# Kernel optimization log

Hardware: AMD Instinct MI355X
Metric: run time of the kernel (lower is better)

Reference implementation:

```python
import jax, jax.numpy as jnp
import numpy as np

B, L, C, N, D, FF, L2 = 1, 2400, 1536, 12, 128, 8960, 512
F_, H_, W_ = 2, 30, 40  # grid: L = F*H*W
EPS = 1e-6


def _rope_table(max_len=1024, d=D):
    # Wan rope_params: three bands of sizes d-4*(d//6), 2*(d//6), 2*(d//6)
    parts = [d - 4 * (d // 6), 2 * (d // 6), 2 * (d // 6)]
    pos = np.arange(max_len, dtype=np.float32)
    cs, ss = [], []
    for dp in parts:
        inv = 1.0 / (10000.0 ** (np.arange(0, dp, 2, dtype=np.float32) / dp))
        ang = np.outer(pos, inv)
        cs.append(np.cos(ang)); ss.append(np.sin(ang))
    return np.stack([np.concatenate(cs, 1), np.concatenate(ss, 1)], -1)  # [1024, d//2, 2]


def setup_inputs() -> dict:
    key = jax.random.key(0)
    ks = iter(jax.random.split(key, 48))
    def rn(shape, s=0.02):
        return jax.random.normal(next(ks), shape, dtype=jnp.float32) * s
    inp = dict(
        x=jax.random.normal(next(ks), (B, L, C), dtype=jnp.float32),
        e=rn((B, 1, 6, C), 0.5),
        context=jax.random.normal(next(ks), (B, L2, C), dtype=jnp.float32),
        freqs=jnp.asarray(_rope_table()),
        seq_lens=jnp.full((B,), L, dtype=jnp.int32),
        context_lens=jnp.full((B,), L2, dtype=jnp.int32),
        grid_sizes=jnp.array([[F_, H_, W_]], dtype=jnp.int32),
        modulation=rn((1, 6, C), 0.5),
    )
    for p in ('sa', 'ca'):
        for w in ('q', 'k', 'v', 'o'):
            inp[f'{p}_{w}_w'] = rn((C, C))
            inp[f'{p}_{w}_b'] = rn((C,))
        inp[f'{p}_nq_w'] = jnp.ones((C,), jnp.float32)
        inp[f'{p}_nk_w'] = jnp.ones((C,), jnp.float32)
    inp['ffn_w1'] = rn((C, FF)); inp['ffn_b1'] = rn((FF,))
    inp['ffn_w2'] = rn((FF, C)); inp['ffn_b2'] = rn((C,))
    return inp


def _rms_norm(x, w):
    v = jnp.mean(jnp.square(x), axis=-1, keepdims=True)
    return x * jax.lax.rsqrt(v + EPS) * w


def _layer_norm(x):
    m = jnp.mean(x, axis=-1, keepdims=True)
    v = jnp.mean(jnp.square(x - m), axis=-1, keepdims=True)
    return (x - m) * jax.lax.rsqrt(v + EPS)


def _apply_rope(x, freqs):
    # x: [B,S,N,D]; freqs: [1024, D//2, 2] (cos, sin). Wan default rope.
    c = D // 2
    p0, p1 = c - 2 * (c // 3), c // 3
    ft = jnp.broadcast_to(freqs[:F_, None, None, :p0], (F_, H_, W_, p0, 2))
    fh = jnp.broadcast_to(freqs[None, :H_, None, p0:p0 + p1], (F_, H_, W_, p1, 2))
    fw = jnp.broadcast_to(freqs[None, None, :W_, p0 + p1:], (F_, H_, W_, c - p0 - p1, 2))
    fr = jnp.concatenate([ft, fh, fw], axis=3).reshape(L, c, 2)
    cos = fr[..., 0][None, :, None, :]  # [1,S,1,c]
    sin = fr[..., 1][None, :, None, :]
    xp = x.reshape(B, x.shape[1], N, c, 2)  # interleaved (real, imag) pairs
    xr, xi = xp[..., 0], xp[..., 1]
    out = jnp.stack([xr * cos - xi * sin, xr * sin + xi * cos], axis=-1)
    return out.reshape(x.shape)


def _attention(q, k, v, k_len):
    # q:[B,Sq,N,D] k,v:[B,Sk,N,D]; dense softmax attention with k_lens mask
    scale = 1.0 / jnp.sqrt(jnp.float32(D))
    scores = jnp.einsum('bqnd,bknd->bnqk', q, k) * scale
    mask = jnp.arange(k.shape[1])[None, None, None, :] < k_len[:, None, None, None]
    scores = jnp.where(mask, scores, -jnp.inf)
    p = jax.nn.softmax(scores, axis=-1)
    return jnp.einsum('bnqk,bknd->bqnd', p, v)


def reference(x, e, context, freqs, seq_lens, context_lens, grid_sizes, modulation,
              sa_q_w, sa_q_b, sa_k_w, sa_k_b, sa_v_w, sa_v_b, sa_o_w, sa_o_b, sa_nq_w, sa_nk_w,
              ca_q_w, ca_q_b, ca_k_w, ca_k_b, ca_v_w, ca_v_b, ca_o_w, ca_o_b, ca_nq_w, ca_nk_w,
              ffn_w1, ffn_b1, ffn_w2, ffn_b2):
    # e: [B,1,6,C] (L1=1, broadcast over L == repeat_e); modulation: [1,6,C]
    em = modulation[None] + e  # [B,1,6,C]
    e0, e1, e2, e3, e4, e5 = (em[:, :, i] for i in range(6))  # each [B,1,C]
    # --- self attention with modulation ---
    h = e0 + _layer_norm(x) * (1.0 + e1)
    q = _rms_norm(h @ sa_q_w + sa_q_b, sa_nq_w).reshape(B, L, N, D)
    k = _rms_norm(h @ sa_k_w + sa_k_b, sa_nk_w).reshape(B, L, N, D)
    v = (h @ sa_v_w + sa_v_b).reshape(B, L, N, D)
    q = _apply_rope(q, freqs)
    k = _apply_rope(k, freqs)
    y = _attention(q, k, v, seq_lens).reshape(B, L, C)
    y = y @ sa_o_w + sa_o_b
    x = x + y * e2
    # --- cross attention (norm3 = Identity, cross_attn_norm=False) ---
    q = _rms_norm(x @ ca_q_w + ca_q_b, ca_nq_w).reshape(B, L, N, D)
    k = _rms_norm(context @ ca_k_w + ca_k_b, ca_nk_w).reshape(B, L2, N, D)
    v = (context @ ca_v_w + ca_v_b).reshape(B, L2, N, D)
    y = _attention(q, k, v, context_lens).reshape(B, L, C)
    x = x + (y @ ca_o_w + ca_o_b)
    # --- FFN with modulation ---
    h = e3 + _layer_norm(x) * (1.0 + e4)
    y = jax.nn.gelu(h @ ffn_w1 + ffn_b1, approximate=True) @ ffn_w2 + ffn_b2
    x = x + y * e5
    return x
```

## Files before the change

### kernel.cpp

```cpp
#include <hip/hip_runtime.h>
#include <cstddef>
#include <cstdint>

#define C_DIM   1536
#define L_SEQ   2400
#define L_CTX   512
#define N_HEADS 12
#define D_HEAD  128
#define FF_DIM  8960
#define F_GRID  2
#define H_GRID  30
#define W_GRID  40
#define EPS_F   1e-6f

#define ROPE_P0 22
#define ROPE_P1 43

typedef __attribute__((ext_vector_type(8))) short short8;
typedef __attribute__((ext_vector_type(4))) float f32x4;

__device__ inline unsigned short f2bf(float f) {
    union { float f; unsigned int u; } v; v.f = f;
    unsigned int r = v.u + 0x7FFF + ((v.u >> 16) & 1);
    return (unsigned short)(r >> 16);
}

#define GL2LDS(gp, lp) \
    __builtin_amdgcn_global_load_lds((const __attribute__((address_space(1))) void*)(gp), \
                                     (__attribute__((address_space(3))) void*)(lp), 16, 0, 0)


__global__ __launch_bounds__(256) void k_embed(const float* __restrict__ mod,
                                               const float* __restrict__ e,
                                               float* __restrict__ ev, int n) {
    int i = blockIdx.x * 256 + threadIdx.x;
    if (i < n) ev[i] = mod[i] + e[i];
}

__global__ __launch_bounds__(256) void k_resid2(const float* __restrict__ a,
                                                const float* __restrict__ b,
                                                const float* __restrict__ ev, int ei,
                                                float* __restrict__ out,
                                                unsigned short* __restrict__ outb, int n) {
    int i = (blockIdx.x * 256 + threadIdx.x) * 2;
    if (i >= n) return;
    int c = i % C_DIM;
    float s0 = 1.f, s1 = 1.f;
    if (ei >= 0) {
        s0 = ev[ei * C_DIM + c];
        s1 = ev[ei * C_DIM + c + 1];
    }
    float2 av = *(const float2*)(a + i);
    float2 bv = *(const float2*)(b + i);
    float o0 = av.x + bv.x * s0;
    float o1 = av.y + bv.y * s1;
    *(float2*)(out + i) = make_float2(o0, o1);
    if (outb) {
        unsigned int pk = (unsigned int)f2bf(o0) | ((unsigned int)f2bf(o1) << 16);
        *(unsigned int*)(outb + i) = pk;
    }
}

__global__ __launch_bounds__(256) void k_tobf(const float* __restrict__ X,
                                              unsigned short* __restrict__ Y, int n) {
    int i = (blockIdx.x * 256 + threadIdx.x) * 2;
    if (i >= n) return;
    float2 v = *(const float2*)(X + i);
    unsigned int pk = (unsigned int)f2bf(v.x) | ((unsigned int)f2bf(v.y) << 16);
    *(unsigned int*)(Y + i) = pk;
}

__global__ __launch_bounds__(256) void k_lnmod_bf16(const float* __restrict__ X,
                                                    const float* __restrict__ ev,
                                                    int i0, int i1,
                                                    unsigned short* __restrict__ H) {
    __shared__ float rs[256];
    __shared__ float rs2[256];
    int row = blockIdx.x, tid = threadIdx.x;
    const float* xr = X + (size_t)row * C_DIM;
    float2 vals[3];
    float s = 0.f, s2 = 0.f;
#pragma unroll
    for (int i = 0; i < 3; ++i) {
        float2 v = *(const float2*)(xr + 2 * (tid + 256 * i));
        vals[i] = v;
        s += v.x + v.y; s2 += v.x * v.x + v.y * v.y;
    }
    rs[tid] = s; rs2[tid] = s2;
    __syncthreads();
    for (int st = 128; st > 0; st >>= 1) {
        if (tid < st) { rs[tid] += rs[tid + st]; rs2[tid] += rs2[tid + st]; }
        __syncthreads();
    }
    float mean = rs[0] * (1.0f / C_DIM);
    float var  = rs2[0] * (1.0f / C_DIM) - mean * mean;
    float rinv = rsqrtf(var + EPS_F);
    const float* E0 = ev + (size_t)i0 * C_DIM;
    const float* E1 = ev + (size_t)i1 * C_DIM;
    unsigned short* hr = H + (size_t)row * C_DIM;
#pragma unroll
    for (int i = 0; i < 3; ++i) {
        int c = 2 * (tid + 256 * i);
        float o0 = E0[c]     + (vals[i].x - mean) * rinv * (1.0f + E1[c]);
        float o1 = E0[c + 1] + (vals[i].y - mean) * rinv * (1.0f + E1[c + 1]);
        unsigned int pk = (unsigned int)f2bf(o0) | ((unsigned int)f2bf(o1) << 16);
        *(unsigned int*)(hr + c) = pk;
    }
}

__global__ __launch_bounds__(256) void k_rms_rope_bf16(const float* __restrict__ X,
                                                       const float* __restrict__ w,
                                                       const float* __restrict__ freqs,
                                                       int do_rope, float outscale,
                                                       unsigned short* __restrict__ Y) {
    __shared__ float rs[256];
    int row = blockIdx.x, tid = threadIdx.x;
    const float* xr = X + (size_t)row * C_DIM;
    float2 vals[3];
    float ss = 0.f;
#pragma unroll
    for (int i = 0; i < 3; ++i) {
        int p = tid + 256 * i;
        float2 v = *(const float2*)(xr + 2 * p);
        vals[i] = v;
        ss += v.x * v.x + v.y * v.y;
    }
    rs[tid] = ss;
    __syncthreads();
    for (int st = 128; st > 0; st >>= 1) {
        if (tid < st) rs[tid] += rs[tid + st];
        __syncthreads();
    }
    float rinv = rsqrtf(rs[0] * (1.0f / C_DIM) + EPS_F);
    int f = row / (H_GRID * W_GRID);
    int rem = row % (H_GRID * W_GRID);
    int hh = rem / W_GRID, ww = rem % W_GRID;
    unsigned short* yr = Y + (size_t)row * C_DIM;
#pragma unroll
    for (int i = 0; i < 3; ++i) {
        int p = tid + 256 * i;
        int c = 2 * p;
        float a = vals[i].x * rinv * w[c];
        float b = vals[i].y * rinv * w[c + 1];
        if (do_rope) {
            int j = p & 63;
            int idx = (j < ROPE_P0) ? f : (j < ROPE_P1) ? hh : ww;
            float cv = freqs[(idx * 64 + j) * 2 + 0];
            float sv = freqs[(idx * 64 + j) * 2 + 1];
            float na = a * cv - b * sv;
            float nb = a * sv + b * cv;
            a = na; b = nb;
        }
        a *= outscale; b *= outscale;
        unsigned int pk = (unsigned int)f2bf(a) | ((unsigned int)f2bf(b) << 16);
        *(unsigned int*)(yr + c) = pk;
    }
}

__global__ __launch_bounds__(256) void k_wt(const float* __restrict__ W,
                                            unsigned short* __restrict__ WT,
                                            int K, int N) {
    __shared__ float tile[32][33];
    int k0 = blockIdx.x * 32, n0 = blockIdx.y * 32;
    int t = threadIdx.x;
    int r = t >> 3, c4 = (t & 7) * 4;
    float4 v = *(const float4*)(W + (size_t)(k0 + r) * N + n0 + c4);
    tile[r][c4 + 0] = v.x; tile[r][c4 + 1] = v.y;
    tile[r][c4 + 2] = v.z; tile[r][c4 + 3] = v.w;
    __syncthreads();
    int n = t >> 3, k4 = (t & 7) * 4;
    uint2 o;
    o.x = (unsigned int)f2bf(tile[k4 + 0][n]) | ((unsigned int)f2bf(tile[k4 + 1][n]) << 16);
    o.y = (unsigned int)f2bf(tile[k4 + 2][n]) | ((unsigned int)f2bf(tile[k4 + 3][n]) << 16);
    *(uint2*)(WT + (size_t)(n0 + n) * K + k0 + k4) = o;
}

__global__ __launch_bounds__(256) void k_vt(const float* __restrict__ V,
                                            unsigned short* __restrict__ Vt, int Lk) {
    __shared__ float tile[32][33];
    int k0 = blockIdx.x * 32, h = blockIdx.y, d0 = blockIdx.z * 32;
    int t = threadIdx.x;
    int k = t >> 3, d4 = (t & 7) * 4;
    float4 v = *(const float4*)(V + (size_t)(k0 + k) * C_DIM + h * D_HEAD + d0 + d4);
    tile[k][d4 + 0] = v.x; tile[k][d4 + 1] = v.y;
    tile[k][d4 + 2] = v.z; tile[k][d4 + 3] = v.w;
    __syncthreads();
    int d = t >> 3, k4 = (t & 7) * 4;
    uint2 o;
    o.x = (unsigned int)f2bf(tile[k4 + 0][d]) | ((unsigned int)f2bf(tile[k4 + 1][d]) << 16);
    o.y = (unsigned int)f2bf(tile[k4 + 2][d]) | ((unsigned int)f2bf(tile[k4 + 3][d]) << 16);
    *(uint2*)(Vt + (size_t)(h * D_HEAD + d0 + d) * Lk + k0 + k4) = o;
}

__global__ __launch_bounds__(256) void k_attn_mfma(const unsigned short* __restrict__ Qb,
                                                   const unsigned short* __restrict__ Kb,
                                                   const unsigned short* __restrict__ Vt,
                                                   unsigned short* __restrict__ O,
                                                   int Lq, int Lk) {
    __shared__ __align__(16) unsigned short Ks[32][136];
    __shared__ __align__(16) unsigned short Vs[128][40];
    __shared__ __align__(16) unsigned short Ps[4][16][40];
    const int tid = threadIdx.x;
    const int w = tid >> 6, lane = tid & 63;
    const int ln = lane & 15, lq = lane >> 4;
    const int h = blockIdx.y;
    const int q0 = blockIdx.x * 64 + w * 16;
    int qrow = q0 + ln; if (qrow >= Lq) qrow = Lq - 1;
    short8 qf[4];
#pragma unroll
    for (int c = 0; c < 4; ++c)
        qf[c] = *(const short8*)(Qb + (size_t)qrow * C_DIM + h * D_HEAD + c * 32 + lq * 8);
    f32x4 oacc[8];
#pragma unroll
    for (int t = 0; t < 8; ++t) oacc[t] = (f32x4){0.f, 0.f, 0.f, 0.f};
    float m_run[4] = {-3e38f, -3e38f, -3e38f, -3e38f};
    float l_run[4] = {0.f, 0.f, 0.f, 0.f};
    const float LOG2E = 1.4426950408889634f;

    for (int kb = 0; kb < Lk; kb += 32) {
        __syncthreads();
#pragma unroll
        for (int i = 0; i < 2; ++i) {
            int id = tid + i * 256;
            int r = id >> 4, c = id & 15;
            *(uint4*)&Ks[r][c * 8] =
                *(const uint4*)(Kb + (size_t)(kb + r) * C_DIM + h * D_HEAD + c * 8);
            int d = id >> 2, c2 = id & 3;
            *(uint4*)&Vs[d][c2 * 8] =
                *(const uint4*)(Vt + (size_t)(h * D_HEAD + d) * Lk + kb + c2 * 8);
        }
        __syncthreads();
        f32x4 c0 = (f32x4){0.f, 0.f, 0.f, 0.f};
        f32x4 c1 = (f32x4){0.f, 0.f, 0.f, 0.f};
#pragma unroll
        for (int c = 0; c < 4; ++c) {
            short8 b0 = *(const short8*)&Ks[ln][c * 32 + lq * 8];
            short8 b1 = *(const short8*)&Ks[16 + ln][c * 32 + lq * 8];
            c0 = __builtin_amdgcn_mfma_f32_16x16x32_bf16(qf[c], b0, c0, 0, 0, 0);
            c1 = __builtin_amdgcn_mfma_f32_16x16x32_bf16(qf[c], b1, c1, 0, 0, 0);
        }
        float alpha[4];
#pragma unroll
        for (int r = 0; r < 4; ++r) {
            float mx = fmaxf(c0[r], c1[r]);
            mx = fmaxf(mx, __shfl_xor(mx, 1));
            mx = fmaxf(mx, __shfl_xor(mx, 2));
            mx = fmaxf(mx, __shfl_xor(mx, 4));
            mx = fmaxf(mx, __shfl_xor(mx, 8));
            float mn = fmaxf(m_run[r], mx);
            alpha[r] = exp2f((m_run[r] - mn) * LOG2E);
            float p0 = exp2f((c0[r] - mn) * LOG2E);
            float p1 = exp2f((c1[r] - mn) * LOG2E);
            float s = p0 + p1;
            s += __shfl_xor(s, 1);
            s += __shfl_xor(s, 2);
            s += __shfl_xor(s, 4);
            s += __shfl_xor(s, 8);
            l_run[r] = l_run[r] * alpha[r] + s;
            m_run[r] = mn;
            Ps[w][lq * 4 + r][ln] = f2bf(p0);
            Ps[w][lq * 4 + r][16 + ln] = f2bf(p1);
        }
#pragma unroll
        for (int t = 0; t < 8; ++t)
#pragma unroll
            for (int r = 0; r < 4; ++r) oacc[t][r] *= alpha[r];
        short8 pa = *(const short8*)&Ps[w][ln][lq * 8];
#pragma unroll
        for (int t = 0; t < 8; ++t) {
            short8 bv = *(const short8*)&Vs[t * 16 + ln][lq * 8];
            oacc[t] = __builtin_amdgcn_mfma_f32_16x16x32_bf16(pa, bv, oacc[t], 0, 0, 0);
        }
    }
    float linv[4];
#pragma unroll
    for (int r = 0; r < 4; ++r) linv[r] = 1.0f / l_run[r];
#pragma unroll
    for (int t = 0; t < 8; ++t)
#pragma unroll
        for (int r = 0; r < 4; ++r) {
            int row = q0 + lq * 4 + r;
            if (row < Lq)
                O[(size_t)row * C_DIM + h * D_HEAD + t * 16 + ln] = f2bf(oacc[t][r] * linv[r]);
        }
}

__global__ __launch_bounds__(256) void k_gemm_bf16(const unsigned short* __restrict__ A,
                                                   const unsigned short* __restrict__ BT,
                                                   const float* __restrict__ bias,
                                                   float* __restrict__ Cf,
                                                   unsigned short* __restrict__ Cb,
                                                   int M, int N, int K, int gelu) {
    __shared__ __align__(16) unsigned short As[128 * 32];
    __shared__ __align__(16) unsigned short Bs[128 * 32];
    const int tid = threadIdx.x;
    const int lane = tid & 63;
    const int w = tid >> 6;
    const int ln = lane & 15, lq = lane >> 4;
    const int wm = w >> 1, wn = w & 1;
    const int bm = blockIdx.y * 128, bn = blockIdx.x * 128;

    int r0 = tid >> 2, c0 = (tid & 3) * 8;
    int ar0 = bm + r0;      if (ar0 >= M) ar0 = M - 1;
    int ar1 = bm + r0 + 64; if (ar1 >= M) ar1 = M - 1;
    const unsigned short* Ag0 = A + (size_t)ar0 * K + c0;
    const unsigned short* Ag1 = A + (size_t)ar1 * K + c0;
    const unsigned short* Bg0 = BT + (size_t)(bn + r0) * K + c0;
    const unsigned short* Bg1 = BT + (size_t)(bn + r0 + 64) * K + c0;
    unsigned short* Al0 = As + tid * 8;
    unsigned short* Al1 = As + 2048 + tid * 8;
    unsigned short* Bl0 = Bs + tid * 8;
    unsigned short* Bl1 = Bs + 2048 + tid * 8;

    f32x4 acc[4][4];
#pragma unroll
    for (int i = 0; i < 4; ++i)
#pragma unroll
        for (int j = 0; j < 4; ++j) acc[i][j] = (f32x4){0.f, 0.f, 0.f, 0.f};

    for (int kb = 0; kb < K; kb += 32) {
        __syncthreads();
        GL2LDS(Ag0 + kb, Al0);
        GL2LDS(Ag1 + kb, Al1);
        GL2LDS(Bg0 + kb, Bl0);
        GL2LDS(Bg1 + kb, Bl1);
        __syncthreads();
        short8 af[4], bf[4];
#pragma unroll
        for (int mi = 0; mi < 4; ++mi)
            af[mi] = *(const short8*)&As[(wm * 64 + mi * 16 + ln) * 32 + lq * 8];
#pragma unroll
        for (int ni = 0; ni < 4; ++ni)
            bf[ni] = *(const short8*)&Bs[(wn * 64 + ni * 16 + ln) * 32 + lq * 8];
#pragma unroll
        for (int mi = 0; mi < 4; ++mi)
#pragma unroll
            for (int ni = 0; ni < 4; ++ni)
                acc[mi][ni] = __builtin_amdgcn_mfma_f32_16x16x32_bf16(af[mi], bf[ni],
                                                                      acc[mi][ni], 0, 0, 0);
    }

#pragma unroll
    for (int ni = 0; ni < 4; ++ni) {
        int col = bn + wn * 64 + ni * 16 + ln;
        float bv = bias[col];
#pragma unroll
        for (int mi = 0; mi < 4; ++mi) {
#pragma unroll
            for (int r = 0; r < 4; ++r) {
                int row = bm + wm * 64 + mi * 16 + lq * 4 + r;
                if (row >= M) continue;
                float v = acc[mi][ni][r] + bv;
                if (gelu) {
                    float u = 0.7978845608028654f * (v + 0.044715f * v * v * v);
                    float ex = __expf(2.f * u);
                    float t = 1.f - 2.f / (ex + 1.f);
                    float g = 0.5f * v * (1.f + t);
                    Cb[(size_t)row * N + col] = f2bf(g);
                } else {
                    Cf[(size_t)row * N + col] = v;
                }
            }
        }
    }
}

extern "C" void kernel_launch(void* const* d_in, const int* in_sizes, int n_in,
                              void* d_out, int out_size, void* d_ws, size_t ws_size,
                              hipStream_t stream) {
    const float* x          = (const float*)d_in[0];
    const float* e          = (const float*)d_in[1];
    const float* context    = (const float*)d_in[2];
    const float* freqs      = (const float*)d_in[3];
    const float* modulation = (const float*)d_in[7];
    const float* sa_q_w = (const float*)d_in[8];
    const float* sa_q_b = (const float*)d_in[9];
    const float* sa_k_w = (const float*)d_in[10];
    const float* sa_k_b = (const float*)d_in[11];
    const float* sa_v_w = (const float*)d_in[12];
    const float* sa_v_b = (const float*)d_in[13];
    const float* sa_o_w = (const float*)d_in[14];
    const float* sa_o_b = (const float*)d_in[15];
    const float* sa_nq  = (const float*)d_in[16];
    const float* sa_nk  = (const float*)d_in[17];
    const float* ca_q_w = (const float*)d_in[18];
    const float* ca_q_b = (const float*)d_in[19];
    const float* ca_k_w = (const float*)d_in[20];
    const float* ca_k_b = (const float*)d_in[21];
    const float* ca_v_w = (const float*)d_in[22];
    const float* ca_v_b = (const float*)d_in[23];
    const float* ca_o_w = (const float*)d_in[24];
    const float* ca_o_b = (const float*)d_in[25];
    const float* ca_nq  = (const float*)d_in[26];
    const float* ca_nk  = (const float*)d_in[27];
    const float* ffn_w1 = (const float*)d_in[28];
    const float* ffn_b1 = (const float*)d_in[29];
    const float* ffn_w2 = (const float*)d_in[30];
    const float* ffn_b2 = (const float*)d_in[31];

    const size_t LC = (size_t)L_SEQ * C_DIM;
    const size_t WMAX = (size_t)C_DIM * FF_DIM;
    char* p = (char*)d_ws;
    float* ev   = (float*)p;            p += 6 * C_DIM * sizeof(float);
    float* Xcur = (float*)p;            p += LC * sizeof(float);
    float* Ebuf = (float*)p;            p += LC * sizeof(float);
    float* Bq   = (float*)p;            p += LC * sizeof(float);
    float* Ck   = (float*)p;            p += LC * sizeof(float);
    float* Dv   = (float*)p;            p += LC * sizeof(float);
    unsigned short* Ab = (unsigned short*)p;  p += LC * sizeof(short);
    unsigned short* Xb = (unsigned short*)p;  p += LC * sizeof(short);
    unsigned short* Qb = (unsigned short*)p;  p += LC * sizeof(short);
    unsigned short* Kb = (unsigned short*)p;  p += LC * sizeof(short);
    unsigned short* Vt = (unsigned short*)p;  p += LC * sizeof(short);
    unsigned short* Ob = (unsigned short*)p;  p += LC * sizeof(short);
    unsigned short* W0 = (unsigned short*)p;  p += WMAX * sizeof(short);
    unsigned short* W1 = (unsigned short*)p;  p += WMAX * sizeof(short);
    unsigned short* Fb = (unsigned short*)Bq;
    unsigned short* Cb = Ab;

    const int nLC = (int)LC;
    const float SCALE = 0.08838834764831845f;
    dim3 blk(256);
    dim3 g_gemm_cc(C_DIM / 128, (L_SEQ + 127) / 128);
    dim3 g_gemm_ctx(C_DIM / 128, L_CTX / 128);
    dim3 g_gemm_ff1(FF_DIM / 128, (L_SEQ + 127) / 128);
    dim3 g_attn((L_SEQ + 63) / 64, N_HEADS);
    dim3 g_vt_s(L_SEQ / 32, N_HEADS, 4);
    dim3 g_vt_c(L_CTX / 32, N_HEADS, 4);
    dim3 g_wt_cc(C_DIM / 32, C_DIM / 32);
    dim3 g_wt_w1(C_DIM / 32, FF_DIM / 32);
    dim3 g_wt_w2(FF_DIM / 32, C_DIM / 32);
    dim3 g_half(nLC / 512);

    k_embed<<<dim3((6 * C_DIM + 255) / 256), blk, 0, stream>>>(modulation, e, ev, 6 * C_DIM);

    k_wt<<<g_wt_cc, blk, 0, stream>>>(sa_q_w, W0, C_DIM, C_DIM);
    k_lnmod_bf16<<<dim3(L_SEQ), blk, 0, stream>>>(x, ev, 0, 1, Ab);
    k_gemm_bf16<<<g_gemm_cc, blk, 0, stream>>>(Ab, W0, sa_q_b, Bq, nullptr, L_SEQ, C_DIM, C_DIM, 0);
    k_wt<<<g_wt_cc, blk, 0, stream>>>(sa_k_w, W1, C_DIM, C_DIM);
    k_rms_rope_bf16<<<dim3(L_SEQ), blk, 0, stream>>>(Bq, sa_nq, freqs, 1, SCALE, Qb);
    k_gemm_bf16<<<g_gemm_cc, blk, 0, stream>>>(Ab, W1, sa_k_b, Ck, nullptr, L_SEQ, C_DIM, C_DIM, 0);
    k_wt<<<g_wt_cc, blk, 0, stream>>>(sa_v_w, W0, C_DIM, C_DIM);
    k_rms_rope_bf16<<<dim3(L_SEQ), blk, 0, stream>>>(Ck, sa_nk, freqs, 1, 1.0f, Kb);
    k_gemm_bf16<<<g_gemm_cc, blk, 0, stream>>>(Ab, W0, sa_v_b, Dv, nullptr, L_SEQ, C_DIM, C_DIM, 0);
    k_wt<<<g_wt_cc, blk, 0, stream>>>(sa_o_w, W1, C_DIM, C_DIM);
    k_vt<<<g_vt_s, blk, 0, stream>>>(Dv, Vt, L_SEQ);
    k_attn_mfma<<<g_attn, blk, 0, stream>>>(Qb, Kb, Vt, Ob, L_SEQ, L_SEQ);
    k_gemm_bf16<<<g_gemm_cc, blk, 0, stream>>>(Ob, W1, sa_o_b, Ebuf, nullptr, L_SEQ, C_DIM, C_DIM, 0);
    k_resid2<<<g_half, blk, 0, stream>>>(x, Ebuf, ev, 2, Xcur, Xb, nLC);

    k_wt<<<g_wt_cc, blk, 0, stream>>>(ca_q_w, W0, C_DIM, C_DIM);
    k_tobf<<<dim3(L_CTX * C_DIM / 512), blk, 0, stream>>>(context, Cb, L_CTX * C_DIM);
    k_gemm_bf16<<<g_gemm_cc, blk, 0, stream>>>(Xb, W0, ca_q_b, Bq, nullptr, L_SEQ, C_DIM, C_DIM, 0);
    k_wt<<<g_wt_cc, blk, 0, stream>>>(ca_k_w, W1, C_DIM, C_DIM);
    k_rms_rope_bf16<<<dim3(L_SEQ), blk, 0, stream>>>(Bq, ca_nq, freqs, 0, SCALE, Qb);
    k_gemm_bf16<<<g_gemm_ctx, blk, 0, stream>>>(Cb, W1, ca_k_b, Ck, nullptr, L_CTX, C_DIM, C_DIM, 0);
    k_wt<<<g_wt_cc, blk, 0, stream>>>(ca_v_w, W0, C_DIM, C_DIM);
    k_rms_rope_bf16<<<dim3(L_CTX), blk, 0, stream>>>(Ck, ca_nk, freqs, 0, 1.0f, Kb);
    k_gemm_bf16<<<g_gemm_ctx, blk, 0, stream>>>(Cb, W0, ca_v_b, Dv, nullptr, L_CTX, C_DIM, C_DIM, 0);
    k_wt<<<g_wt_cc, blk, 0, stream>>>(ca_o_w, W1, C_DIM, C_DIM);
    k_vt<<<g_vt_c, blk, 0, stream>>>(Dv, Vt, L_CTX);
    k_attn_mfma<<<g_attn, blk, 0, stream>>>(Qb, Kb, Vt, Ob, L_SEQ, L_CTX);
    k_gemm_bf16<<<g_gemm_cc, blk, 0, stream>>>(Ob, W1, ca_o_b, Ebuf, nullptr, L_SEQ, C_DIM, C_DIM, 0);
    k_resid2<<<g_half, blk, 0, stream>>>(Xcur, Ebuf, (const float*)nullptr, -1, Xcur, nullptr, nLC);

    k_wt<<<g_wt_w1, blk, 0, stream>>>(ffn_w1, W0, C_DIM, FF_DIM);
    k_lnmod_bf16<<<dim3(L_SEQ), blk, 0, stream>>>(Xcur, ev, 3, 4, Ab);
    k_gemm_bf16<<<g_gemm_ff1, blk, 0, stream>>>(Ab, W0, ffn_b1, nullptr, Fb, L_SEQ, FF_DIM, C_DIM, 1);
    k_wt<<<g_wt_w2, blk, 0, stream>>>(ffn_w2, W1, FF_DIM, C_DIM);
    k_gemm_bf16<<<g_gemm_cc, blk, 0, stream>>>(Fb, W1, ffn_b2, Ebuf, nullptr, L_SEQ, C_DIM, FF_DIM, 0);
    k_resid2<<<g_half, blk, 0, stream>>>(Xcur, Ebuf, ev, 5, (float*)d_out, nullptr, nLC);
}
```

Baseline: 1.235 ms.

## Fuse QKV projections into wide GEMMs and split-K narrow GEMMs with atomics

Self-attention Q/K/V weights are transposed into one concatenated matrix so a single 4608-wide GEMM replaces three launches, and context K/V likewise become one 3072-wide GEMM. Narrow 1536-wide projections and the FFN down-projection are split along K into 4 slices, with outputs pre-initialised with bias and accumulated via float atomicAdd. The aim is more blocks in flight on the many CUs for the small 12x19 grids. The cost is extra bias-init passes, atomic traffic, and non-deterministic summation order.

```diff
diff --git a/kernel.cpp b/kernel.cpp
--- a/kernel.cpp
+++ b/kernel.cpp
@@ -35,6 +35,26 @@
                                                float* __restrict__ ev, int n) {
     int i = blockIdx.x * 256 + threadIdx.x;
     if (i < n) ev[i] = mod[i] + e[i];
+}
+
+__global__ __launch_bounds__(256) void k_catbias(float* __restrict__ dst,
+                                                 const float* __restrict__ b0,
+                                                 const float* __restrict__ b1,
+                                                 const float* __restrict__ b2,
+                                                 int ne, int n) {
+    int i = blockIdx.x * 256 + threadIdx.x;
+    if (i >= n) return;
+    const float* s = (i < ne) ? b0 : (i < 2 * ne) ? b1 : b2;
+    dst[i] = s[i % ne];
+}
+
+__global__ __launch_bounds__(256) void k_initbias(float* __restrict__ C,
+                                                  const float* __restrict__ bias,
+                                                  int n, int N) {
+    int i4 = (blockIdx.x * 256 + threadIdx.x) * 4;
+    if (i4 >= n) return;
+    int col = i4 % N;
+    *(float4*)(C + i4) = *(const float4*)(bias + col);
 }
 
 __global__ __launch_bounds__(256) void k_resid2(const float* __restrict__ a,
@@ -112,10 +132,11 @@
                                                        const float* __restrict__ w,
                                                        const float* __restrict__ freqs,
                                                        int do_rope, float outscale,
-                                                       unsigned short* __restrict__ Y) {
+                                                       unsigned short* __restrict__ Y,
+                                                       int ldx) {
     __shared__ float rs[256];
     int row = blockIdx.x, tid = threadIdx.x;
-    const float* xr = X + (size_t)row * C_DIM;
+    const float* xr = X + (size_t)row * ldx;
     float2 vals[3];
     float ss = 0.f;
 #pragma unroll
@@ -176,12 +197,12 @@
 }
 
 __global__ __launch_bounds__(256) void k_vt(const float* __restrict__ V,
-                                            unsigned short* __restrict__ Vt, int Lk) {
+                                            unsigned short* __restrict__ Vt, int Lk, int ldv) {
     __shared__ float tile[32][33];
     int k0 = blockIdx.x * 32, h = blockIdx.y, d0 = blockIdx.z * 32;
     int t = threadIdx.x;
     int k = t >> 3, d4 = (t & 7) * 4;
-    float4 v = *(const float4*)(V + (size_t)(k0 + k) * C_DIM + h * D_HEAD + d0 + d4);
+    float4 v = *(const float4*)(V + (size_t)(k0 + k) * ldv + h * D_HEAD + d0 + d4);
     tile[k][d4 + 0] = v.x; tile[k][d4 + 1] = v.y;
     tile[k][d4 + 2] = v.z; tile[k][d4 + 3] = v.w;
     __syncthreads();
@@ -290,7 +311,8 @@
                                                    const float* __restrict__ bias,
                                                    float* __restrict__ Cf,
                                                    unsigned short* __restrict__ Cb,
-                                                   int M, int N, int K, int gelu) {
+                                                   int M, int N, int K, int Kc,
+                                                   int gelu, int atomic) {
     __shared__ __align__(16) unsigned short As[128 * 32];
     __shared__ __align__(16) unsigned short Bs[128 * 32];
     const int tid = threadIdx.x;
@@ -299,6 +321,7 @@
     const int ln = lane & 15, lq = lane >> 4;
     const int wm = w >> 1, wn = w & 1;
     const int bm = blockIdx.y * 128, bn = blockIdx.x * 128;
+    const int kb0 = blockIdx.z * Kc;
 
     int r0 = tid >> 2, c0 = (tid & 3) * 8;
     int ar0 = bm + r0;      if (ar0 >= M) ar0 = M - 1;
@@ -318,7 +341,7 @@
 #pragma unroll
         for (int j = 0; j < 4; ++j) acc[i][j] = (f32x4){0.f, 0.f, 0.f, 0.f};
 
-    for (int kb = 0; kb < K; kb += 32) {
+    for (int kb = kb0; kb < kb0 + Kc; kb += 32) {
         __syncthreads();
         GL2LDS(Ag0 + kb, Al0);
         GL2LDS(Ag1 + kb, Al1);
@@ -343,22 +366,23 @@
 #pragma unroll
     for (int ni = 0; ni < 4; ++ni) {
         int col = bn + wn * 64 + ni * 16 + ln;
-        float bv = bias[col];
+        float bv = atomic ? 0.f : bias[col];
 #pragma unroll
         for (int mi = 0; mi < 4; ++mi) {
 #pragma unroll
             for (int r = 0; r < 4; ++r) {
                 int row = bm + wm * 64 + mi * 16 + lq * 4 + r;
                 if (row >= M) continue;
-                float v = acc[mi][ni][r] + bv;
-                if (gelu) {
+                if (atomic) {
+                    atomicAdd(Cf + (size_t)row * N + col, acc[mi][ni][r]);
+                } else if (gelu) {
+                    float v = acc[mi][ni][r] + bv;
                     float u = 0.7978845608028654f * (v + 0.044715f * v * v * v);
                     float ex = __expf(2.f * u);
                     float t = 1.f - 2.f / (ex + 1.f);
-                    float g = 0.5f * v * (1.f + t);
-                    Cb[(size_t)row * N + col] = f2bf(g);
+                    Cb[(size_t)row * N + col] = f2bf(0.5f * v * (1.f + t));
                 } else {
-                    Cf[(size_t)row * N + col] = v;
+                    Cf[(size_t)row * N + col] = acc[mi][ni][r] + bv;
                 }
             }
         }
@@ -402,11 +426,10 @@
     const size_t WMAX = (size_t)C_DIM * FF_DIM;
     char* p = (char*)d_ws;
     float* ev   = (float*)p;            p += 6 * C_DIM * sizeof(float);
+    float* Bcat = (float*)p;            p += 3 * C_DIM * sizeof(float);
     float* Xcur = (float*)p;            p += LC * sizeof(float);
     float* Ebuf = (float*)p;            p += LC * sizeof(float);
-    float* Bq   = (float*)p;            p += LC * sizeof(float);
-    float* Ck   = (float*)p;            p += LC * sizeof(float);
-    float* Dv   = (float*)p;            p += LC * sizeof(float);
+    float* QKV  = (float*)p;            p += 3 * LC * sizeof(float);
     unsigned short* Ab = (unsigned short*)p;  p += LC * sizeof(short);
     unsigned short* Xb = (unsigned short*)p;  p += LC * sizeof(short);
     unsigned short* Qb = (unsigned short*)p;  p += LC * sizeof(short);
@@ -415,15 +438,17 @@
     unsigned short* Ob = (unsigned short*)p;  p += LC * sizeof(short);
     unsigned short* W0 = (unsigned short*)p;  p += WMAX * sizeof(short);
     unsigned short* W1 = (unsigned short*)p;  p += WMAX * sizeof(short);
-    unsigned short* Fb = (unsigned short*)Bq;
-    unsigned short* Cb = Ab;
+    unsigned short* Fb = (unsigned short*)QKV;
+    float* Pq    = QKV;
+    float* ctxKV = QKV + LC;
 
     const int nLC = (int)LC;
     const float SCALE = 0.08838834764831845f;
     dim3 blk(256);
-    dim3 g_gemm_cc(C_DIM / 128, (L_SEQ + 127) / 128);
-    dim3 g_gemm_ctx(C_DIM / 128, L_CTX / 128);
-    dim3 g_gemm_ff1(FF_DIM / 128, (L_SEQ + 127) / 128);
+    dim3 g_qkv(4608 / 128, 19, 1);
+    dim3 g_proj_s4(C_DIM / 128, 19, 4);
+    dim3 g_ctxkv_s4(3072 / 128, L_CTX / 128, 4);
+    dim3 g_ff1(FF_DIM / 128, 19, 1);
     dim3 g_attn((L_SEQ + 63) / 64, N_HEADS);
     dim3 g_vt_s(L_SEQ / 32, N_HEADS, 4);
     dim3 g_vt_c(L_CTX / 32, N_HEADS, 4);
@@ -431,43 +456,58 @@
     dim3 g_wt_w1(C_DIM / 32, FF_DIM / 32);
     dim3 g_wt_w2(FF_DIM / 32, C_DIM / 32);
     dim3 g_half(nLC / 512);
+    dim3 g_init_cc(nLC / 1024);
+    dim3 g_init_kv(L_CTX * 3072 / 1024);
 
     k_embed<<<dim3((6 * C_DIM + 255) / 256), blk, 0, stream>>>(modulation, e, ev, 6 * C_DIM);
 
+    k_catbias<<<dim3((3 * C_DIM + 255) / 256), blk, 0, stream>>>(Bcat, sa_q_b, sa_k_b, sa_v_b,
+                                                                 C_DIM, 3 * C_DIM);
     k_wt<<<g_wt_cc, blk, 0, stream>>>(sa_q_w, W0, C_DIM, C_DIM);
+    k_wt<<<g_wt_cc, blk, 0, stream>>>(sa_k_w, W0 + (size_t)C_DIM * C_DIM, C_DIM, C_DIM);
+    k_wt<<<g_wt_cc, blk, 0, stream>>>(sa_v_w, W0 + (size_t)2 * C_DIM * C_DIM, C_DIM, C_DIM);
     k_lnmod_bf16<<<dim3(L_SEQ), blk, 0, stream>>>(x, ev, 0, 1, Ab);
-    k_gemm_bf16<<<g_gemm_cc, blk, 0, stream>>>(Ab, W0, sa_q_b, Bq, nullptr, L_SEQ, C_DIM, C_DIM, 0);
-    k_wt<<<g_wt_cc, blk, 0, stream>>>(sa_k_w, W1, C_DIM, C_DIM);
-    k_rms_rope_bf16<<<dim3(L_SEQ), blk, 0, stream>>>(Bq, sa_nq, freqs, 1, SCALE, Qb);
-    k_gemm_bf16<<<g_gemm_cc, blk, 0, stream>>>(Ab, W1, sa_k_b, Ck, nullptr, L_SEQ, C_DIM, C_DIM, 0);
-    k_wt<<<g_wt_cc, blk, 0, stream>>>(sa_v_w, W0, C_DIM, C_DIM);
-    k_rms_rope_bf16<<<dim3(L_SEQ), blk, 0, stream>>>(Ck, sa_nk, freqs, 1, 1.0f, Kb);
-    k_gemm_bf16<<<g_gemm_cc, blk, 0, stream>>>(Ab, W0, sa_v_b, Dv, nullptr, L_SEQ, C_DIM, C_DIM, 0);
+    k_gemm_bf16<<<g_qkv, blk, 0, stream>>>(Ab, W0, Bcat, QKV, nullptr,
+                                           L_SEQ, 4608, C_DIM, C_DIM, 0, 0);
     k_wt<<<g_wt_cc, blk, 0, stream>>>(sa_o_w, W1, C_DIM, C_DIM);
-    k_vt<<<g_vt_s, blk, 0, stream>>>(Dv, Vt, L_SEQ);
+    k_rms_rope_bf16<<<dim3(L_SEQ), blk, 0, stream>>>(QKV, sa_nq, freqs, 1, SCALE, Qb, 4608);
+    k_rms_rope_bf16<<<dim3(L_SEQ), blk, 0, stream>>>(QKV + C_DIM, sa_nk, freqs, 1, 1.0f, Kb, 4608);
+    k_vt<<<g_vt_s, blk, 0, stream>>>(QKV + 2 * C_DIM, Vt, L_SEQ, 4608);
     k_attn_mfma<<<g_attn, blk, 0, stream>>>(Qb, Kb, Vt, Ob, L_SEQ, L_SEQ);
-    k_gemm_bf16<<<g_gemm_cc, blk, 0, stream>>>(Ob, W1, sa_o_b, Ebuf, nullptr, L_SEQ, C_DIM, C_DIM, 0);
+    k_initbias<<<g_init_cc, blk, 0, stream>>>(Ebuf, sa_o_b, nLC, C_DIM);
+    k_gemm_bf16<<<g_proj_s4, blk, 0, stream>>>(Ob, W1, nullptr, Ebuf, nullptr,
+                                               L_SEQ, C_DIM, C_DIM, 384, 0, 1);
     k_resid2<<<g_half, blk, 0, stream>>>(x, Ebuf, ev, 2, Xcur, Xb, nLC);
 
     k_wt<<<g_wt_cc, blk, 0, stream>>>(ca_q_w, W0, C_DIM, C_DIM);
-    k_tobf<<<dim3(L_CTX * C_DIM / 512), blk, 0, stream>>>(context, Cb, L_CTX * C_DIM);
-    k_gemm_bf16<<<g_gemm_cc, blk, 0, stream>>>(Xb, W0, ca_q_b, Bq, nullptr, L_SEQ, C_DIM, C_DIM, 0);
     k_wt<<<g_wt_cc, blk, 0, stream>>>(ca_k_w, W1, C_DIM, C_DIM);
-    k_rms_rope_bf16<<<dim3(L_SEQ), blk, 0, stream>>>(Bq, ca_nq, freqs, 0, SCALE, Qb);
-    k_gemm_bf16<<<g_gemm_ctx, blk, 0, stream>>>(Cb, W1, ca_k_b, Ck, nullptr, L_CTX, C_DIM, C_DIM, 0);
-    k_wt<<<g_wt_cc, blk, 0, stream>>>(ca_v_w, W0, C_DIM, C_DIM);
-    k_rms_rope_bf16<<<dim3(L_CTX), blk, 0, stream>>>(Ck, ca_nk, freqs, 0, 1.0f, Kb);
-    k_gemm_bf16<<<g_gemm_ctx, blk, 0, stream>>>(Cb, W0, ca_v_b, Dv, nullptr, L_CTX, C_DIM, C_DIM, 0);
-    k_wt<<<g_wt_cc, blk, 0, stream>>>(ca_o_w, W1, C_DIM, C_DIM);
-    k_vt<<<g_vt_c, blk, 0, stream>>>(Dv, Vt, L_CTX);
+    k_wt<<<g_wt_cc, blk, 0, stream>>>(ca_v_w, W1 + (size_t)C_DIM * C_DIM, C_DIM, C_DIM);
+    k_tobf<<<dim3(L_CTX * C_DIM / 512), blk, 0, stream>>>(context, Ab, L_CTX * C_DIM);
+    k_catbias<<<dim3((2 * C_DIM + 255) / 256), blk, 0, stream>>>(Bcat, ca_k_b, ca_v_b, nullptr,
+                                                                 C_DIM, 2 * C_DIM);
+    k_initbias<<<g_init_cc, blk, 0, stream>>>(Pq, ca_q_b, nLC, C_DIM);
+    k_gemm_bf16<<<g_proj_s4, blk, 0, stream>>>(Xb, W0, nullptr, Pq, nullptr,
+                                               L_SEQ, C_DIM, C_DIM, 384, 0, 1);
+    k_initbias<<<g_init_kv, blk, 0, stream>>>(ctxKV, Bcat, L_CTX * 3072, 3072);
+    k_gemm_bf16<<<g_ctxkv_s4, blk, 0, stream>>>(Ab, W1, nullptr, ctxKV, nullptr,
+                                                L_CTX, 3072, C_DIM, 384, 0, 1);
+    k_rms_rope_bf16<<<dim3(L_SEQ), blk, 0, stream>>>(Pq, ca_nq, freqs, 0, SCALE, Qb, C_DIM);
+    k_rms_rope_bf16<<<dim3(L_CTX), blk, 0, stream>>>(ctxKV, ca_nk, freqs, 0, 1.0f, Kb, 3072);
+    k_vt<<<g_vt_c, blk, 0, stream>>>(ctxKV + C_DIM, Vt, L_CTX, 3072);
     k_attn_mfma<<<g_attn, blk, 0, stream>>>(Qb, Kb, Vt, Ob, L_SEQ, L_CTX);
-    k_gemm_bf16<<<g_gemm_cc, blk, 0, stream>>>(Ob, W1, ca_o_b, Ebuf, nullptr, L_SEQ, C_DIM, C_DIM, 0);
+    k_wt<<<g_wt_cc, blk, 0, stream>>>(ca_o_w, W0, C_DIM, C_DIM);
+    k_initbias<<<g_init_cc, blk, 0, stream>>>(Ebuf, ca_o_b, nLC, C_DIM);
+    k_gemm_bf16<<<g_proj_s4, blk, 0, stream>>>(Ob, W0, nullptr, Ebuf, nullptr,
+                                               L_SEQ, C_DIM, C_DIM, 384, 0, 1);
     k_resid2<<<g_half, blk, 0, stream>>>(Xcur, Ebuf, (const float*)nullptr, -1, Xcur, nullptr, nLC);
 
-    k_wt<<<g_wt_w1, blk, 0, stream>>>(ffn_w1, W0, C_DIM, FF_DIM);
+    k_wt<<<g_wt_w1, blk, 0, stream>>>(ffn_w1, W1, C_DIM, FF_DIM);
     k_lnmod_bf16<<<dim3(L_SEQ), blk, 0, stream>>>(Xcur, ev, 3, 4, Ab);
-    k_gemm_bf16<<<g_gemm_ff1, blk, 0, stream>>>(Ab, W0, ffn_b1, nullptr, Fb, L_SEQ, FF_DIM, C_DIM, 1);
-    k_wt<<<g_wt_w2, blk, 0, stream>>>(ffn_w2, W1, FF_DIM, C_DIM);
-    k_gemm_bf16<<<g_gemm_cc, blk, 0, stream>>>(Fb, W1, ffn_b2, Ebuf, nullptr, L_SEQ, C_DIM, FF_DIM, 0);
+    k_gemm_bf16<<<g_ff1, blk, 0, stream>>>(Ab, W1, ffn_b1, nullptr, Fb,
+                                           L_SEQ, FF_DIM, C_DIM, C_DIM, 1, 0);
+    k_wt<<<g_wt_w2, blk, 0, stream>>>(ffn_w2, W0, FF_DIM, C_DIM);
+    k_initbias<<<g_init_cc, blk, 0, stream>>>(Ebuf, ffn_b2, nLC, C_DIM);
+    k_gemm_bf16<<<g_proj_s4, blk, 0, stream>>>(Fb, W0, nullptr, Ebuf, nullptr,
+                                               L_SEQ, C_DIM, FF_DIM, 2240, 0, 1);
     k_resid2<<<g_half, blk, 0, stream>>>(Xcur, Ebuf, ev, 5, (float*)d_out, nullptr, nLC);
 }
```

After: 1.122 ms. 1.1x faster.
